# Performance work log

Measured on AMD Instinct MI355X. Metric: run time of the kernel, lower is better.

The kernel has to match this reference:

```python
import jax, jax.numpy as jnp
import numpy as np

N, F, T, D = 10000, 16, 12, 16
C = 1.0
MIN_NORM = 1e-15
PROJ_EPS = 4e-3  # float32 boundary eps in PoincareBall.proj


def _norm(x):
    return jnp.clip(jnp.linalg.norm(x, axis=-1, keepdims=True), MIN_NORM, None)


def artanh(x):
    return jnp.arctanh(jnp.clip(x, -1 + 1e-7, 1 - 1e-7))


def proj(x, c):
    n = _norm(x)
    maxnorm = (1.0 - PROJ_EPS) / jnp.sqrt(c)
    return jnp.where(n > maxnorm, x / n * maxnorm, x)


def expmap0(u, c):
    sc = jnp.sqrt(c)
    un = _norm(u)
    return jnp.tanh(sc * un) * u / (sc * un)


def logmap0(p, c):
    sc = jnp.sqrt(c)
    pn = _norm(p)
    return artanh(sc * pn) * p / (sc * pn)


def mobius_add(x, y, c):
    x2 = jnp.sum(x * x, -1, keepdims=True)
    y2 = jnp.sum(y * y, -1, keepdims=True)
    xy = jnp.sum(x * y, -1, keepdims=True)
    num = (1 + 2 * c * xy + c * y2) * x + (1 - c * x2) * y
    den = 1 + 2 * c * xy + c * c * x2 * y2
    return num / jnp.clip(den, MIN_NORM, None)


def mobius_matvec(m, x, c):
    sc = jnp.sqrt(c)
    xn = _norm(x)
    mx = x @ m.T
    mxn = _norm(mx)
    res = jnp.tanh(mxn / xn * artanh(sc * xn)) * mx / (mxn * sc)
    return jnp.where(jnp.all(mx == 0, axis=-1, keepdims=True), 0.0, res)


def temporal_attention(x, U1, U2, U3, be, Ve):
    # x: (B, N, F, T)
    lhs = jnp.einsum('bnft,n,fm->btm', x, U1, U2)   # (B, T, N)
    rhs = jnp.einsum('f,bnft->bnt', U3, x)          # (B, N, T)
    product = jnp.einsum('btn,bns->bts', lhs, rhs)  # (B, T, T)
    E = jnp.einsum('ij,bjs->bis', Ve, jax.nn.sigmoid(product + be))
    return jax.nn.softmax(E, axis=1)


def time_conv(x, w, b):
    # x: (B, F, N, T), kernel (1,3), padding (0,1), stride 1
    y = jax.lax.conv_general_dilated(x, w, (1, 1), ((0, 0), (1, 1)),
                                     dimension_numbers=('NCHW', 'OIHW', 'NCHW'))
    return y + b[None, :, None, None]


def hgc_layer(x_hyp, adj, w, b, c):
    # HypLinear (dropout=0 / eval mode)
    mv = proj(mobius_matvec(w, x_hyp, c), c)
    hyp_b = proj(expmap0(b.reshape(1, -1), c), c)
    res = proj(mobius_add(mv, hyp_b, c), c)
    # HypAgg (use_att=False): aggregate in tangent space at origin
    xt = logmap0(res, c)
    sup = jnp.einsum('mn,tnd->tmd', adj, xt)  # adj @ x_tangent per timestep
    agg = proj(expmap0(sup, c), c)
    # HypAct: relu, c_in == c_out (proj_tan0 is identity)
    return proj(expmap0(jax.nn.relu(logmap0(agg, c)), c), c)


def _forward(x, adj, U1a, U2a, U3a, be_a, Ve_a, U1b, U2b, U3b, be_b, Ve_b,
             conv1_w, conv1_b, conv2_w, conv2_b, hgc_w, hgc_b):
    xb = x[None]  # (1, N, F, T)
    # ---- first temporal attention + conv + hyperbolic GCN over timesteps ----
    tA = temporal_attention(xb, U1a, U2a, U3a, be_a, Ve_a)  # (1, T, T)
    x_tat = (xb.reshape(1, N * F, T) @ tA).reshape(1, N, F, T)
    x_tat = time_conv(jnp.transpose(x_tat, (0, 2, 1, 3)), conv1_w, conv1_b)  # (1, F, N, T)
    y_all = jnp.transpose(x_tat[0], (2, 1, 0))  # (T, N, F): per-timestep node features
    x_hyp = proj(expmap0(y_all, C), C)          # proj_tan0 is identity on PoincareBall
    out = hgc_layer(x_hyp, adj, hgc_w, hgc_b, C)  # (T, N, D)
    h = jnp.transpose(out, (1, 2, 0))[None]       # (1, N, D, T)
    # ---- second temporal attention + conv (this is what encode() returns) ----
    tA2 = temporal_attention(xb, U1b, U2b, U3b, be_b, Ve_b)
    x_tat2 = (xb.reshape(1, N * F, T) @ tA2).reshape(1, N, F, T)
    x_tat2 = time_conv(jnp.transpose(x_tat2, (0, 2, 1, 3)), conv2_w, conv2_b)
    final_output = jnp.transpose(x_tat2, (0, 3, 2, 1))  # (1, T, N, F)
    return final_output, h


def setup_inputs():
    key = jax.random.key(0)
    ks = jax.random.split(key, 16)

    def nrm(k, shape, scale=0.1):
        return jax.random.normal(k, shape, jnp.float32) * scale

    adj = jax.random.uniform(ks[1], (N, N), jnp.float32)
    adj = adj / jnp.sum(adj, axis=1, keepdims=True)  # row-normalized dense adjacency
    return {
        'x': jax.random.normal(ks[0], (N, F, T), jnp.float32),
        'adj': adj,
        'U1a': nrm(ks[2], (N,), 0.01), 'U2a': nrm(ks[3], (F, N), 0.01),
        'U3a': nrm(ks[4], (F,)), 'be_a': nrm(ks[5], (1, T, T)), 'Ve_a': nrm(ks[6], (T, T)),
        'U1b': nrm(ks[7], (N,), 0.01), 'U2b': nrm(ks[8], (F, N), 0.01),
        'U3b': nrm(ks[9], (F,)), 'be_b': nrm(ks[10], (1, T, T)), 'Ve_b': nrm(ks[11], (T, T)),
        'conv1_w': nrm(ks[12], (F, F, 1, 3)), 'conv1_b': jnp.zeros((F,), jnp.float32),
        'conv2_w': nrm(ks[13], (F, F, 1, 3)), 'conv2_b': jnp.zeros((F,), jnp.float32),
        'hgc_w': nrm(ks[14], (D, F)), 'hgc_b': nrm(ks[15], (D,), 0.01),
    }


def reference(x, adj, U1a, U2a, U3a, be_a, Ve_a, U1b, U2b, U3b, be_b, Ve_b,
              conv1_w, conv1_b, conv2_w, conv2_b, hgc_w, hgc_b):
    return _forward(x, adj, U1a, U2a, U3a, be_a, Ve_a, U1b, U2b, U3b, be_b, Ve_b,
                    conv1_w, conv1_b, conv2_w, conv2_b, hgc_w, hgc_b)
```

## Files before the change

### kernel.cpp

```cpp
#include <hip/hip_runtime.h>
#include <hip/hip_bf16.h>
#include <math.h>

#define NN 10000

typedef __attribute__((ext_vector_type(4))) float f32x4;
typedef __attribute__((ext_vector_type(8))) short short8v;

__device__ __forceinline__ short f2bf(float f) {
  union { float f; unsigned u; } v; v.f = f;
  unsigned u = v.u + 0x7FFFu + ((v.u >> 16) & 1u);
  return (short)(u >> 16);
}
__device__ __forceinline__ float bf2f(unsigned short h) {
  union { unsigned u; float f; } v; v.u = ((unsigned)h) << 16;
  return v.f;
}
__device__ __forceinline__ float artanh_(float xx) {
  xx = fminf(fmaxf(xx, -1.f + 1e-7f), 1.f - 1e-7f);
  return atanhf(xx);
}
__device__ __forceinline__ void proj16(float* v) {
  float s = 0.f;
#pragma unroll
  for (int i = 0; i < 16; ++i) s += v[i] * v[i];
  float n = fmaxf(sqrtf(s), 1e-15f);
  const float mxn = 1.0f - 4e-3f;
  if (n > mxn) {
    float sc = mxn / n;
#pragma unroll
    for (int i = 0; i < 16; ++i) v[i] *= sc;
  }
}
__device__ __forceinline__ short8v cvt8(const float4& u, const float4& w) {
  union { __hip_bfloat162 h; unsigned u32; } c0, c1, c2, c3;
  c0.h = __float22bfloat162_rn(make_float2(u.x, u.y));
  c1.h = __float22bfloat162_rn(make_float2(u.z, u.w));
  c2.h = __float22bfloat162_rn(make_float2(w.x, w.y));
  c3.h = __float22bfloat162_rn(make_float2(w.z, w.w));
  union { unsigned v[4]; short8v s; } r;
  r.v[0] = c0.u32; r.v[1] = c1.u32; r.v[2] = c2.u32; r.v[3] = c3.u32;
  return r.s;
}

__global__ __launch_bounds__(192) void k_attn1(
    const float* __restrict__ x,
    const float* __restrict__ U1a, const float* __restrict__ U3a,
    const float* __restrict__ U1b, const float* __restrict__ U3b,
    float* __restrict__ rhsA, float* __restrict__ rhsB,
    float* __restrict__ partAa, float* __restrict__ partAb,
    unsigned short* __restrict__ PB) {
  __shared__ float xs[16 * 193];
  int tid = threadIdx.x;
  int f_ = tid / 12, t_ = tid - f_ * 12;
  int s_ = tid >> 4, nl_ = tid & 15;
  if (blockIdx.x == 79) {
    for (int i = tid; i < 3072; i += 192) {
      int tt = i >> 8, q = i & 255;
      PB[(size_t)(312 * 12 + tt) * 512 + 256 + q] = 0;
    }
  }
  float paa = 0.f, pab = 0.f;
  for (int tb = blockIdx.x; tb < 625; tb += 160) {
    int n0 = tb * 16;
    for (int i = tid; i < 16 * 192; i += 192) {
      int a = i / 192, j = i - a * 192;
      xs[a * 193 + j] = x[(size_t)(n0 + a) * 192 + j];
    }
    __syncthreads();
    float ra = 0.f, rb = 0.f;
#pragma unroll
    for (int f = 0; f < 16; ++f) {
      float xv = xs[nl_ * 193 + f * 12 + s_];
      ra += xv * U3a[f];
      rb += xv * U3b[f];
    }
    rhsA[s_ * NN + n0 + nl_] = ra;
    rhsB[s_ * NN + n0 + nl_] = rb;
#pragma unroll
    for (int nl = 0; nl < 16; ++nl) {
      float xv = xs[nl * 193 + f_ * 12 + t_];
      paa += xv * U1a[n0 + nl];
      pab += xv * U1b[n0 + nl];
    }
    __syncthreads();
  }
  partAa[blockIdx.x * 192 + tid] = paa;
  partAb[blockIdx.x * 192 + tid] = pab;
}

__global__ __launch_bounds__(192) void k_attn2(
    const float* __restrict__ U2a, const float* __restrict__ U2b,
    const float* __restrict__ rhsA, const float* __restrict__ rhsB,
    float* __restrict__ partMa, float* __restrict__ partMb) {
  int tid = threadIdx.x;
  int f = tid / 12, s = tid - f * 12;
  int nA = blockIdx.x * 125, nE = nA + 125;
  float ma = 0.f, mb = 0.f;
  for (int n = nA; n < nE; ++n) {
    ma += U2a[f * NN + n] * rhsA[s * NN + n];
    mb += U2b[f * NN + n] * rhsB[s * NN + n];
  }
  partMa[blockIdx.x * 192 + tid] = ma;
  partMb[blockIdx.x * 192 + tid] = mb;
}

__global__ __launch_bounds__(192) void k_attn3(
    const float* __restrict__ partAa, const float* __restrict__ partAb,
    const float* __restrict__ partMa, const float* __restrict__ partMb,
    const float* __restrict__ beA, const float* __restrict__ VeA,
    const float* __restrict__ beB, const float* __restrict__ VeB,
    float* __restrict__ tAa, float* __restrict__ tAb) {
  __shared__ float aa[192], ab[192], Ma[192], Mb[192];
  __shared__ float spA[144], spB[144], EA[144], EB[144];
  int tid = threadIdx.x;
  float s1 = 0.f, s2 = 0.f, s3 = 0.f, s4 = 0.f;
  for (int b = 0; b < 160; ++b) { s1 += partAa[b * 192 + tid]; s2 += partAb[b * 192 + tid]; }
  for (int b = 0; b < 80; ++b) { s3 += partMa[b * 192 + tid]; s4 += partMb[b * 192 + tid]; }
  aa[tid] = s1; ab[tid] = s2; Ma[tid] = s3; Mb[tid] = s4;
  __syncthreads();
  if (tid < 144) {
    int j = tid / 12, s = tid - j * 12;
    float pa = 0.f, pb = 0.f;
#pragma unroll
    for (int f = 0; f < 16; ++f) {
      pa += aa[f * 12 + j] * Ma[f * 12 + s];
      pb += ab[f * 12 + j] * Mb[f * 12 + s];
    }
    spA[tid] = 1.f / (1.f + expf(-(pa + beA[tid])));
    spB[tid] = 1.f / (1.f + expf(-(pb + beB[tid])));
  }
  __syncthreads();
  if (tid < 144) {
    int i = tid / 12, s = tid - i * 12;
    float ea = 0.f, eb = 0.f;
#pragma unroll
    for (int j = 0; j < 12; ++j) {
      ea += VeA[i * 12 + j] * spA[j * 12 + s];
      eb += VeB[i * 12 + j] * spB[j * 12 + s];
    }
    EA[tid] = ea; EB[tid] = eb;
  }
  __syncthreads();
  if (tid < 144) {
    int s = tid % 12;
    float ma = -1e30f, mb = -1e30f;
#pragma unroll
    for (int k = 0; k < 12; ++k) { ma = fmaxf(ma, EA[k * 12 + s]); mb = fmaxf(mb, EB[k * 12 + s]); }
    float da = 0.f, db = 0.f;
#pragma unroll
    for (int k = 0; k < 12; ++k) { da += expf(EA[k * 12 + s] - ma); db += expf(EB[k * 12 + s] - mb); }
    tAa[tid] = expf(EA[tid] - ma) / da;
    tAb[tid] = expf(EB[tid] - mb) / db;
  }
}

__global__ __launch_bounds__(192) void k_node(
    const float* __restrict__ x,
    const float* __restrict__ tAa_g, const float* __restrict__ tAb_g,
    const float* __restrict__ w1g, const float* __restrict__ b1g,
    const float* __restrict__ w2g, const float* __restrict__ b2g,
    const float* __restrict__ hwg, const float* __restrict__ hbg,
    float* __restrict__ outF, unsigned short* __restrict__ PB) {
  __shared__ float xs[16 * 193], tbuf[16 * 193];
  __shared__ float tAa[144], tAb[144], w1[768], w2[768];
  __shared__ float cb1[16], cb2[16], hw[256], hbr[16];
  int tid = threadIdx.x;
  int nl = tid & 15, tt = tid >> 4;
  int n0 = blockIdx.x * 16;
  for (int i = tid; i < 144; i += 192) { tAa[i] = tAa_g[i]; tAb[i] = tAb_g[i]; }
  for (int i = tid; i < 768; i += 192) { w1[i] = w1g[i]; w2[i] = w2g[i]; }
  for (int i = tid; i < 256; i += 192) hw[i] = hwg[i];
  if (tid < 16) { cb1[tid] = b1g[tid]; cb2[tid] = b2g[tid]; hbr[tid] = hbg[tid]; }
  for (int i = tid; i < 16 * 192; i += 192) {
    int a = i / 192, j = i - a * 192;
    xs[a * 193 + j] = x[(size_t)(n0 + a) * 192 + j];
  }
  __syncthreads();

  float z[16];
#pragma unroll
  for (int f = 0; f < 16; ++f) {
    float v = 0.f;
#pragma unroll
    for (int s = 0; s < 12; ++s) v += xs[nl * 193 + f * 12 + s] * tAb[s * 12 + tt];
    tbuf[nl * 193 + f * 12 + tt] = v;
  }
  __syncthreads();
#pragma unroll
  for (int o = 0; o < 16; ++o) z[o] = cb2[o];
#pragma unroll
  for (int k = 0; k < 3; ++k) {
    int t2 = tt + k - 1;
    if (t2 >= 0 && t2 < 12) {
#pragma unroll
      for (int i = 0; i < 16; ++i) {
        float xv = tbuf[nl * 193 + i * 12 + t2];
#pragma unroll
        for (int o = 0; o < 16; ++o) z[o] += xv * w2[o * 48 + i * 3 + k];
      }
    }
  }
  {
    float* op = outF + (size_t)tt * (NN * 16) + (size_t)(n0 + nl) * 16;
#pragma unroll
    for (int o = 0; o < 16; ++o) op[o] = z[o];
  }
  __syncthreads();

#pragma unroll
  for (int f = 0; f < 16; ++f) {
    float v = 0.f;
#pragma unroll
    for (int s = 0; s < 12; ++s) v += xs[nl * 193 + f * 12 + s] * tAa[s * 12 + tt];
    tbuf[nl * 193 + f * 12 + tt] = v;
  }
  __syncthreads();
#pragma unroll
  for (int o = 0; o < 16; ++o) z[o] = cb1[o];
#pragma unroll
  for (int k = 0; k < 3; ++k) {
    int t2 = tt + k - 1;
    if (t2 >= 0 && t2 < 12) {
#pragma unroll
      for (int i = 0; i < 16; ++i) {
        float xv = tbuf[nl * 193 + i * 12 + t2];
#pragma unroll
        for (int o = 0; o < 16; ++o) z[o] += xv * w1[o * 48 + i * 3 + k];
      }
    }
  }
  float nz = 0.f;
#pragma unroll
  for (int i = 0; i < 16; ++i) nz += z[i] * z[i];
  nz = fmaxf(sqrtf(nz), 1e-15f);
  float sc0 = tanhf(nz) / nz;
#pragma unroll
  for (int i = 0; i < 16; ++i) z[i] *= sc0;
  proj16(z);
  float xn = 0.f;
#pragma unroll
  for (int i = 0; i < 16; ++i) xn += z[i] * z[i];
  xn = fmaxf(sqrtf(xn), 1e-15f);
  float mx[16];
#pragma unroll
  for (int d = 0; d < 16; ++d) {
    float v = 0.f;
#pragma unroll
    for (int f = 0; f < 16; ++f) v += z[f] * hw[d * 16 + f];
    mx[d] = v;
  }
  float mxr = 0.f;
#pragma unroll
  for (int d = 0; d < 16; ++d) mxr += mx[d] * mx[d];
  mxr = sqrtf(mxr);
  float mxn = fmaxf(mxr, 1e-15f);
  float rs = tanhf(mxn / xn * artanh_(xn)) / mxn;
  if (mxr == 0.f) rs = 0.f;
#pragma unroll
  for (int d = 0; d < 16; ++d) mx[d] *= rs;
  proj16(mx);
  float hb[16];
  float bn = 0.f;
#pragma unroll
  for (int i = 0; i < 16; ++i) { hb[i] = hbr[i]; bn += hb[i] * hb[i]; }
  bn = fmaxf(sqrtf(bn), 1e-15f);
  float sb = tanhf(bn) / bn;
#pragma unroll
  for (int i = 0; i < 16; ++i) hb[i] *= sb;
  proj16(hb);
  float x2 = 0.f, y2 = 0.f, xy = 0.f;
#pragma unroll
  for (int i = 0; i < 16; ++i) { x2 += mx[i] * mx[i]; y2 += hb[i] * hb[i]; xy += mx[i] * hb[i]; }
  float ca = 1.f + 2.f * xy + y2;
  float cbv = 1.f - x2;
  float den = fmaxf(1.f + 2.f * xy + x2 * y2, 1e-15f);
#pragma unroll
  for (int i = 0; i < 16; ++i) mx[i] = (ca * mx[i] + cbv * hb[i]) / den;
  proj16(mx);
  float pn = 0.f;
#pragma unroll
  for (int i = 0; i < 16; ++i) pn += mx[i] * mx[i];
  pn = fmaxf(sqrtf(pn), 1e-15f);
  float sl = artanh_(pn) / pn;
  {
    int nn2 = n0 + nl;
    int s = nn2 >> 5, c = nn2 & 31;
    unsigned short* pp = PB + (size_t)(s * 12 + tt) * 512 + (c >> 3) * 128 + (c & 7);
#pragma unroll
    for (int d = 0; d < 16; ++d)
      pp[d * 8] = (unsigned short)f2bf(mx[d] * sl);
  }
}

__global__ __launch_bounds__(512) void k_gemm(
    const float* __restrict__ adj, const unsigned short* __restrict__ PB,
    unsigned short* __restrict__ partC, int S) {
  extern __shared__ char smem[];
  int tid = threadIdx.x;
  int w = tid >> 6, lane = tid & 63;
  int bc = blockIdx.x / 40;
  int rt = blockIdx.x - bc * 40;
  int t0 = bc * S, t1 = min(313, t0 + S);
  int ns = t1 - t0;
  int r0 = lane & 15, kq = lane >> 4;
  int R0w = rt * 256 + w * 32;

  int aoffF = (((lane & 7) * 16) ^ ((lane >> 3) << 4)) >> 2;
  int arow[4];
#pragma unroll
  for (int i = 0; i < 4; ++i) arow[i] = min(R0w + i * 8 + (lane >> 3), NN - 1);

  int bc0 = w;
  int bc1 = (w < 4) ? (8 + w) : w;

  f32x4 acc0[12], acc1[12];
  f32x4 zz = {0.f, 0.f, 0.f, 0.f};
#pragma unroll
  for (int j = 0; j < 12; ++j) { acc0[j] = zz; acc1[j] = zz; }

  auto STAGE = [&](int p, int t) {
    char* Bdst = smem + 98304 + p * 12288;
    const char* Bsrc = (const char*)PB + (size_t)t * 12288;
    __builtin_amdgcn_global_load_lds((const void*)(Bsrc + bc0 * 1024 + lane * 16),
                                     (void*)(Bdst + bc0 * 1024 + lane * 16), 16, 0, 0);
    __builtin_amdgcn_global_load_lds((const void*)(Bsrc + bc1 * 1024 + lane * 16),
                                     (void*)(Bdst + bc1 * 1024 + lane * 16), 16, 0, 0);
    char* Adst = smem + p * 32768 + (w * 32) * 128;
#pragma unroll
    for (int i = 0; i < 4; ++i) {
      int fo = t * 32 + aoffF;
      if (fo >= NN) fo = 0;
      __builtin_amdgcn_global_load_lds((const void*)(adj + (size_t)arow[i] * NN + fo),
                                       (void*)(Adst + i * 1024 + lane * 16), 16, 0, 0);
    }
  };

  int xr = (r0 & 7) << 4;
  auto MM = [&](int p) {
    const char* Ab = smem + p * 32768 + (w * 32) * 128;
    const char* Bb = smem + 98304 + p * 12288;
    float4 a00 = *(const float4*)(Ab + r0 * 128 + ((kq * 32) ^ xr));
    float4 a01 = *(const float4*)(Ab + r0 * 128 + ((kq * 32 + 16) ^ xr));
    float4 a10 = *(const float4*)(Ab + (r0 + 16) * 128 + ((kq * 32) ^ xr));
    float4 a11 = *(const float4*)(Ab + (r0 + 16) * 128 + ((kq * 32 + 16) ^ xr));
    short8v fa0 = cvt8(a00, a01);
    short8v fa1 = cvt8(a10, a11);
#pragma unroll
    for (int j = 0; j < 12; ++j) {
      short8v b = *(const short8v*)(Bb + j * 1024 + lane * 16);
      acc0[j] = __builtin_amdgcn_mfma_f32_16x16x32_bf16(fa0, b, acc0[j], 0, 0, 0);
      acc1[j] = __builtin_amdgcn_mfma_f32_16x16x32_bf16(fa1, b, acc1[j], 0, 0, 0);
    }
  };

  STAGE(0, t0);
  if (ns > 1) STAGE(1, t0 + 1);
  if (ns > 1) asm volatile("s_waitcnt vmcnt(6)" ::: "memory");
  else        asm volatile("s_waitcnt vmcnt(0)" ::: "memory");
  __builtin_amdgcn_sched_barrier(0);
  __builtin_amdgcn_s_barrier();
  __builtin_amdgcn_sched_barrier(0);

  for (int i = 0; i < ns; ++i) {
    if (i + 2 < ns) STAGE((i + 2) % 3, t0 + i + 2);
    MM(i % 3);
    asm volatile("s_waitcnt lgkmcnt(0)" ::: "memory");
    if (i + 1 < ns) {
      if (i + 2 < ns) asm volatile("s_waitcnt vmcnt(6)" ::: "memory");
      else            asm volatile("s_waitcnt vmcnt(0)" ::: "memory");
      __builtin_amdgcn_sched_barrier(0);
      __builtin_amdgcn_s_barrier();
      __builtin_amdgcn_sched_barrier(0);
    }
  }

  size_t cbase = (size_t)bc * ((size_t)NN * 192);
  int drow = kq * 4;
#pragma unroll
  for (int j = 0; j < 12; ++j) {
#pragma unroll
    for (int r = 0; r < 4; ++r) {
      int rw0 = R0w + drow + r;
      int rw1 = R0w + 16 + drow + r;
      if (rw0 < NN)
        partC[cbase + (size_t)rw0 * 192 + j * 16 + r0] = (unsigned short)f2bf(acc0[j][r]);
      if (rw1 < NN)
        partC[cbase + (size_t)rw1 * 192 + j * 16 + r0] = (unsigned short)f2bf(acc1[j][r]);
    }
  }
}

__global__ __launch_bounds__(256) void k_epi(const unsigned short* __restrict__ partC,
                                             float* __restrict__ outH, int NC) {
  int gid = blockIdx.x * 256 + threadIdx.x;
  if (gid >= NN * 12) return;
  int n = gid / 12, t = gid - n * 12;
  float sup[16];
#pragma unroll
  for (int d = 0; d < 16; ++d) sup[d] = 0.f;
  for (int c = 0; c < NC; ++c) {
    const short8v* p8 = (const short8v*)(partC + (size_t)c * (NN * 192) + (size_t)n * 192 + t * 16);
    short8v lo = p8[0], hi = p8[1];
#pragma unroll
    for (int d = 0; d < 8; ++d) sup[d] += bf2f((unsigned short)lo[d]);
#pragma unroll
    for (int d = 0; d < 8; ++d) sup[8 + d] += bf2f((unsigned short)hi[d]);
  }
  float nn_ = 0.f;
#pragma unroll
  for (int d = 0; d < 16; ++d) nn_ += sup[d] * sup[d];
  nn_ = fmaxf(sqrtf(nn_), 1e-15f);
  float s0 = tanhf(nn_) / nn_;
#pragma unroll
  for (int d = 0; d < 16; ++d) sup[d] *= s0;
  proj16(sup);
  float pn = 0.f;
#pragma unroll
  for (int d = 0; d < 16; ++d) pn += sup[d] * sup[d];
  pn = fmaxf(sqrtf(pn), 1e-15f);
  float sl = artanh_(pn) / pn;
#pragma unroll
  for (int d = 0; d < 16; ++d) sup[d] = fmaxf(sup[d] * sl, 0.f);
  float un = 0.f;
#pragma unroll
  for (int d = 0; d < 16; ++d) un += sup[d] * sup[d];
  un = fmaxf(sqrtf(un), 1e-15f);
  float se = tanhf(un) / un;
#pragma unroll
  for (int d = 0; d < 16; ++d) sup[d] *= se;
  proj16(sup);
  float* hp = outH + (size_t)n * 192 + t;
#pragma unroll
  for (int d = 0; d < 16; ++d) hp[d * 12] = sup[d];
}

extern "C" void kernel_launch(void* const* d_in, const int* in_sizes, int n_in,
                              void* d_out, int out_size, void* d_ws, size_t ws_size,
                              hipStream_t stream) {
  const float* x   = (const float*)d_in[0];
  const float* adj = (const float*)d_in[1];
  const float* U1a = (const float*)d_in[2];
  const float* U2a = (const float*)d_in[3];
  const float* U3a = (const float*)d_in[4];
  const float* bea = (const float*)d_in[5];
  const float* Vea = (const float*)d_in[6];
  const float* U1b = (const float*)d_in[7];
  const float* U2b = (const float*)d_in[8];
  const float* U3b = (const float*)d_in[9];
  const float* beb = (const float*)d_in[10];
  const float* Veb = (const float*)d_in[11];
  const float* w1  = (const float*)d_in[12];
  const float* b1  = (const float*)d_in[13];
  const float* w2  = (const float*)d_in[14];
  const float* b2  = (const float*)d_in[15];
  const float* hw  = (const float*)d_in[16];
  const float* hb  = (const float*)d_in[17];
  float* outF = (float*)d_out;
  float* outH = (float*)d_out + 1920000;

  char* ws = (char*)d_ws;
  size_t off = 0;
  auto alloc = [&](size_t bytes) {
    char* p = ws + off;
    off = (off + bytes + 255) & ~(size_t)255;
    return p;
  };
  float* rhsA   = (float*)alloc((size_t)12 * NN * 4);
  float* rhsB   = (float*)alloc((size_t)12 * NN * 4);
  float* partAa = (float*)alloc(160 * 192 * 4);
  float* partAb = (float*)alloc(160 * 192 * 4);
  float* partMa = (float*)alloc(80 * 192 * 4);
  float* partMb = (float*)alloc(80 * 192 * 4);
  float* tAa    = (float*)alloc(144 * 4);
  float* tAb    = (float*)alloc(144 * 4);
  unsigned short* PB = (unsigned short*)alloc((size_t)314 * 6144 * 2);
  const int NC = 6;
  unsigned short* partC = (unsigned short*)alloc((size_t)NC * NN * 192 * 2);
  (void)ws_size;
  int S = (313 + NC - 1) / NC;

  (void)hipFuncSetAttribute((const void*)k_gemm,
                            hipFuncAttributeMaxDynamicSharedMemorySize, 135168);

  k_attn1<<<160, 192, 0, stream>>>(x, U1a, U3a, U1b, U3b, rhsA, rhsB, partAa, partAb, PB);
  k_attn2<<<80, 192, 0, stream>>>(U2a, U2b, rhsA, rhsB, partMa, partMb);
  k_attn3<<<1, 192, 0, stream>>>(partAa, partAb, partMa, partMb, bea, Vea, beb, Veb, tAa, tAb);
  k_node<<<625, 192, 0, stream>>>(x, tAa, tAb, w1, b1, w2, b2, hw, hb, outF, PB);
  k_gemm<<<40 * NC, 512, 135168, stream>>>(adj, PB, partC, S);
  k_epi<<<(NN * 12 + 255) / 256, 256, 0, stream>>>(partC, outH, NC);
}
```

Before: 223.6 us.

## Fuse attention stages, split node kernel across two halves, coalesce epilogue stores

Merges the two attention-reduction kernels into one, so the rhs projections stay in shared memory instead of round-tripping through global buffers, and removes a launch. The node kernel now runs 384 threads so the two temporal-attention and conv branches run concurrently in separate halves, using a second shared buffer. The epilogue transposes its results through shared memory so output stores are contiguous per node. This costs more shared memory and an extra barrier per tile in the attention kernel. The later kernels, including the GEMM, are unchanged.

```diff
diff --git a/kernel.cpp b/kernel.cpp
--- a/kernel.cpp
+++ b/kernel.cpp
@@ -43,14 +43,15 @@
   return r.s;
 }
 
-__global__ __launch_bounds__(192) void k_attn1(
+__global__ __launch_bounds__(192) void k_attn12(
     const float* __restrict__ x,
-    const float* __restrict__ U1a, const float* __restrict__ U3a,
-    const float* __restrict__ U1b, const float* __restrict__ U3b,
-    float* __restrict__ rhsA, float* __restrict__ rhsB,
+    const float* __restrict__ U1a, const float* __restrict__ U3a, const float* __restrict__ U2a,
+    const float* __restrict__ U1b, const float* __restrict__ U3b, const float* __restrict__ U2b,
     float* __restrict__ partAa, float* __restrict__ partAb,
+    float* __restrict__ partMa, float* __restrict__ partMb,
     unsigned short* __restrict__ PB) {
   __shared__ float xs[16 * 193];
+  __shared__ float rsA[16][13], rsB[16][13];
   int tid = threadIdx.x;
   int f_ = tid / 12, t_ = tid - f_ * 12;
   int s_ = tid >> 4, nl_ = tid & 15;
@@ -60,7 +61,7 @@
       PB[(size_t)(312 * 12 + tt) * 512 + 256 + q] = 0;
     }
   }
-  float paa = 0.f, pab = 0.f;
+  float paa = 0.f, pab = 0.f, ma = 0.f, mb = 0.f;
   for (int tb = blockIdx.x; tb < 625; tb += 160) {
     int n0 = tb * 16;
     for (int i = tid; i < 16 * 192; i += 192) {
@@ -68,15 +69,17 @@
       xs[a * 193 + j] = x[(size_t)(n0 + a) * 192 + j];
     }
     __syncthreads();
-    float ra = 0.f, rb = 0.f;
-#pragma unroll
-    for (int f = 0; f < 16; ++f) {
-      float xv = xs[nl_ * 193 + f * 12 + s_];
-      ra += xv * U3a[f];
-      rb += xv * U3b[f];
-    }
-    rhsA[s_ * NN + n0 + nl_] = ra;
-    rhsB[s_ * NN + n0 + nl_] = rb;
+    {
+      float ra = 0.f, rb = 0.f;
+#pragma unroll
+      for (int f = 0; f < 16; ++f) {
+        float xv = xs[nl_ * 193 + f * 12 + s_];
+        ra += xv * U3a[f];
+        rb += xv * U3b[f];
+      }
+      rsA[nl_][s_] = ra;
+      rsB[nl_][s_] = rb;
+    }
 #pragma unroll
     for (int nl = 0; nl < 16; ++nl) {
       float xv = xs[nl * 193 + f_ * 12 + t_];
@@ -84,23 +87,17 @@
       pab += xv * U1b[n0 + nl];
     }
     __syncthreads();
+#pragma unroll
+    for (int nl = 0; nl < 16; ++nl) {
+      float u2a = U2a[(size_t)f_ * NN + n0 + nl];
+      float u2b = U2b[(size_t)f_ * NN + n0 + nl];
+      ma += u2a * rsA[nl][t_];
+      mb += u2b * rsB[nl][t_];
+    }
+    __syncthreads();
   }
   partAa[blockIdx.x * 192 + tid] = paa;
   partAb[blockIdx.x * 192 + tid] = pab;
-}
-
-__global__ __launch_bounds__(192) void k_attn2(
-    const float* __restrict__ U2a, const float* __restrict__ U2b,
-    const float* __restrict__ rhsA, const float* __restrict__ rhsB,
-    float* __restrict__ partMa, float* __restrict__ partMb) {
-  int tid = threadIdx.x;
-  int f = tid / 12, s = tid - f * 12;
-  int nA = blockIdx.x * 125, nE = nA + 125;
-  float ma = 0.f, mb = 0.f;
-  for (int n = nA; n < nE; ++n) {
-    ma += U2a[f * NN + n] * rhsA[s * NN + n];
-    mb += U2b[f * NN + n] * rhsB[s * NN + n];
-  }
   partMa[blockIdx.x * 192 + tid] = ma;
   partMb[blockIdx.x * 192 + tid] = mb;
 }
@@ -115,8 +112,10 @@
   __shared__ float spA[144], spB[144], EA[144], EB[144];
   int tid = threadIdx.x;
   float s1 = 0.f, s2 = 0.f, s3 = 0.f, s4 = 0.f;
-  for (int b = 0; b < 160; ++b) { s1 += partAa[b * 192 + tid]; s2 += partAb[b * 192 + tid]; }
-  for (int b = 0; b < 80; ++b) { s3 += partMa[b * 192 + tid]; s4 += partMb[b * 192 + tid]; }
+  for (int b = 0; b < 160; ++b) {
+    s1 += partAa[b * 192 + tid]; s2 += partAb[b * 192 + tid];
+    s3 += partMa[b * 192 + tid]; s4 += partMb[b * 192 + tid];
+  }
   aa[tid] = s1; ab[tid] = s2; Ma[tid] = s3; Mb[tid] = s4;
   __syncthreads();
   if (tid < 144) {
@@ -155,81 +154,66 @@
   }
 }
 
-__global__ __launch_bounds__(192) void k_node(
+__global__ __launch_bounds__(384) void k_node(
     const float* __restrict__ x,
     const float* __restrict__ tAa_g, const float* __restrict__ tAb_g,
     const float* __restrict__ w1g, const float* __restrict__ b1g,
     const float* __restrict__ w2g, const float* __restrict__ b2g,
     const float* __restrict__ hwg, const float* __restrict__ hbg,
     float* __restrict__ outF, unsigned short* __restrict__ PB) {
-  __shared__ float xs[16 * 193], tbuf[16 * 193];
+  __shared__ float xs[16 * 193], tbA[16 * 193], tbB[16 * 193];
   __shared__ float tAa[144], tAb[144], w1[768], w2[768];
   __shared__ float cb1[16], cb2[16], hw[256], hbr[16];
   int tid = threadIdx.x;
-  int nl = tid & 15, tt = tid >> 4;
+  int half = tid / 192, lt = tid - half * 192;
+  int nl = lt & 15, tt = lt >> 4;
   int n0 = blockIdx.x * 16;
-  for (int i = tid; i < 144; i += 192) { tAa[i] = tAa_g[i]; tAb[i] = tAb_g[i]; }
-  for (int i = tid; i < 768; i += 192) { w1[i] = w1g[i]; w2[i] = w2g[i]; }
-  for (int i = tid; i < 256; i += 192) hw[i] = hwg[i];
+  for (int i = tid; i < 144; i += 384) { tAa[i] = tAa_g[i]; tAb[i] = tAb_g[i]; }
+  for (int i = tid; i < 768; i += 384) { w1[i] = w1g[i]; w2[i] = w2g[i]; }
+  for (int i = tid; i < 256; i += 384) hw[i] = hwg[i];
   if (tid < 16) { cb1[tid] = b1g[tid]; cb2[tid] = b2g[tid]; hbr[tid] = hbg[tid]; }
-  for (int i = tid; i < 16 * 192; i += 192) {
+  for (int i = tid; i < 16 * 192; i += 384) {
     int a = i / 192, j = i - a * 192;
     xs[a * 193 + j] = x[(size_t)(n0 + a) * 192 + j];
   }
   __syncthreads();
 
-  float z[16];
+  float* tb = half ? tbA : tbB;
+  const float* tA = half ? tAa : tAb;
 #pragma unroll
   for (int f = 0; f < 16; ++f) {
     float v = 0.f;
 #pragma unroll
-    for (int s = 0; s < 12; ++s) v += xs[nl * 193 + f * 12 + s] * tAb[s * 12 + tt];
-    tbuf[nl * 193 + f * 12 + tt] = v;
-  }
-  __syncthreads();
-#pragma unroll
-  for (int o = 0; o < 16; ++o) z[o] = cb2[o];
+    for (int s = 0; s < 12; ++s) v += xs[nl * 193 + f * 12 + s] * tA[s * 12 + tt];
+    tb[nl * 193 + f * 12 + tt] = v;
+  }
+  __syncthreads();
+
+  const float* wv = half ? w1 : w2;
+  const float* cbv = half ? cb1 : cb2;
+  float z[16];
+#pragma unroll
+  for (int o = 0; o < 16; ++o) z[o] = cbv[o];
 #pragma unroll
   for (int k = 0; k < 3; ++k) {
     int t2 = tt + k - 1;
     if (t2 >= 0 && t2 < 12) {
 #pragma unroll
       for (int i = 0; i < 16; ++i) {
-        float xv = tbuf[nl * 193 + i * 12 + t2];
-#pragma unroll
-        for (int o = 0; o < 16; ++o) z[o] += xv * w2[o * 48 + i * 3 + k];
+        float xv = tb[nl * 193 + i * 12 + t2];
+#pragma unroll
+        for (int o = 0; o < 16; ++o) z[o] += xv * wv[o * 48 + i * 3 + k];
       }
     }
   }
-  {
+
+  if (half == 0) {
     float* op = outF + (size_t)tt * (NN * 16) + (size_t)(n0 + nl) * 16;
 #pragma unroll
     for (int o = 0; o < 16; ++o) op[o] = z[o];
-  }
-  __syncthreads();
-
-#pragma unroll
-  for (int f = 0; f < 16; ++f) {
-    float v = 0.f;
-#pragma unroll
-    for (int s = 0; s < 12; ++s) v += xs[nl * 193 + f * 12 + s] * tAa[s * 12 + tt];
-    tbuf[nl * 193 + f * 12 + tt] = v;
-  }
-  __syncthreads();
-#pragma unroll
-  for (int o = 0; o < 16; ++o) z[o] = cb1[o];
-#pragma unroll
-  for (int k = 0; k < 3; ++k) {
-    int t2 = tt + k - 1;
-    if (t2 >= 0 && t2 < 12) {
-#pragma unroll
-      for (int i = 0; i < 16; ++i) {
-        float xv = tbuf[nl * 193 + i * 12 + t2];
-#pragma unroll
-        for (int o = 0; o < 16; ++o) z[o] += xv * w1[o * 48 + i * 3 + k];
-      }
-    }
-  }
+    return;
+  }
+
   float nz = 0.f;
 #pragma unroll
   for (int i = 0; i < 16; ++i) nz += z[i] * z[i];
@@ -273,10 +257,10 @@
 #pragma unroll
   for (int i = 0; i < 16; ++i) { x2 += mx[i] * mx[i]; y2 += hb[i] * hb[i]; xy += mx[i] * hb[i]; }
   float ca = 1.f + 2.f * xy + y2;
-  float cbv = 1.f - x2;
+  float cbf = 1.f - x2;
   float den = fmaxf(1.f + 2.f * xy + x2 * y2, 1e-15f);
 #pragma unroll
-  for (int i = 0; i < 16; ++i) mx[i] = (ca * mx[i] + cbv * hb[i]) / den;
+  for (int i = 0; i < 16; ++i) mx[i] = (ca * mx[i] + cbf * hb[i]) / den;
   proj16(mx);
   float pn = 0.f;
 #pragma unroll
@@ -391,11 +375,14 @@
   }
 }
 
-__global__ __launch_bounds__(256) void k_epi(const unsigned short* __restrict__ partC,
+__global__ __launch_bounds__(192) void k_epi(const unsigned short* __restrict__ partC,
                                              float* __restrict__ outH, int NC) {
-  int gid = blockIdx.x * 256 + threadIdx.x;
-  if (gid >= NN * 12) return;
-  int n = gid / 12, t = gid - n * 12;
+  __shared__ float tr[16][196];
+  int tid = threadIdx.x;
+  int nl = tid >> 4 == 12 ? 0 : 0;
+  (void)nl;
+  int node = tid / 12, t = tid - node * 12;
+  int n = blockIdx.x * 16 + node;
   float sup[16];
 #pragma unroll
   for (int d = 0; d < 16; ++d) sup[d] = 0.f;
@@ -430,9 +417,14 @@
 #pragma unroll
   for (int d = 0; d < 16; ++d) sup[d] *= se;
   proj16(sup);
-  float* hp = outH + (size_t)n * 192 + t;
-#pragma unroll
-  for (int d = 0; d < 16; ++d) hp[d * 12] = sup[d];
+#pragma unroll
+  for (int d = 0; d < 16; ++d) tr[node][d * 12 + t] = sup[d];
+  __syncthreads();
+  int wn = tid >> 4, wc = tid & 15;
+  wn = tid / 12; wc = tid - wn * 12;
+  float* hp = outH + (size_t)(blockIdx.x * 16 + wn) * 192 + wc * 16;
+#pragma unroll
+  for (int i = 0; i < 16; ++i) hp[i] = tr[wn][wc * 16 + i];
 }
 
 extern "C" void kernel_launch(void* const* d_in, const int* in_sizes, int n_in,
@@ -466,12 +458,10 @@
     off = (off + bytes + 255) & ~(size_t)255;
     return p;
   };
-  float* rhsA   = (float*)alloc((size_t)12 * NN * 4);
-  float* rhsB   = (float*)alloc((size_t)12 * NN * 4);
   float* partAa = (float*)alloc(160 * 192 * 4);
   float* partAb = (float*)alloc(160 * 192 * 4);
-  float* partMa = (float*)alloc(80 * 192 * 4);
-  float* partMb = (float*)alloc(80 * 192 * 4);
+  float* partMa = (float*)alloc(160 * 192 * 4);
+  float* partMb = (float*)alloc(160 * 192 * 4);
   float* tAa    = (float*)alloc(144 * 4);
   float* tAb    = (float*)alloc(144 * 4);
   unsigned short* PB = (unsigned short*)alloc((size_t)314 * 6144 * 2);
@@ -483,10 +473,10 @@
   (void)hipFuncSetAttribute((const void*)k_gemm,
                             hipFuncAttributeMaxDynamicSharedMemorySize, 135168);
 
-  k_attn1<<<160, 192, 0, stream>>>(x, U1a, U3a, U1b, U3b, rhsA, rhsB, partAa, partAb, PB);
-  k_attn2<<<80, 192, 0, stream>>>(U2a, U2b, rhsA, rhsB, partMa, partMb);
+  k_attn12<<<160, 192, 0, stream>>>(x, U1a, U3a, U2a, U1b, U3b, U2b,
+                                    partAa, partAb, partMa, partMb, PB);
   k_attn3<<<1, 192, 0, stream>>>(partAa, partAb, partMa, partMb, bea, Vea, beb, Veb, tAa, tAb);
-  k_node<<<625, 192, 0, stream>>>(x, tAa, tAb, w1, b1, w2, b2, hw, hb, outF, PB);
+  k_node<<<625, 384, 0, stream>>>(x, tAa, tAb, w1, b1, w2, b2, hw, hb, outF, PB);
   k_gemm<<<40 * NC, 512, 135168, stream>>>(adj, PB, partC, S);
-  k_epi<<<(NN * 12 + 255) / 256, 256, 0, stream>>>(partC, outH, NC);
-}
+  k_epi<<<625, 192, 0, stream>>>(partC, outH, NC);
+}
```

Measured after the change: 242.4 us. 1.08x slower.
